# Kernel tuning notes

Hardware: AMD Instinct MI355X
Metric: run time of the kernel (lower is better)

The kernel has to match this reference:

```python
import jax, jax.numpy as jnp
import numpy as np

NUM_BLOCKS = 10  # labels 1..10; label 0 = background
EPS = 1e-6


def setup_inputs() -> dict:
    key = jax.random.key(0)
    k1, k2, k3 = jax.random.split(key, 3)
    shape = (8, 128, 128, 128)
    inp = jax.random.uniform(k1, shape, dtype=jnp.float32)
    tgt = jax.random.uniform(k2, shape, dtype=jnp.float32)
    blk = jax.random.randint(k3, shape, 0, NUM_BLOCKS + 1, dtype=jnp.int32)
    return {"input": inp, "target": tgt, "block": blk}


def _dice_from_sums(intersect, input_area, target_area):
    # intersect/areas: [B, NUM_BLOCKS]; faithful to cal_dice_loss per block.
    denom = input_area + target_area + 2.0 * EPS
    batch_loss = 1.0 - 2.0 * intersect / denom          # [B, NUM_BLOCKS]
    batch_loss = jnp.where(target_area == 0, 0.0, batch_loss)
    valid = jnp.sum(target_area != 0, axis=0).astype(batch_loss.dtype)  # [NUM_BLOCKS]
    return jnp.sum(batch_loss, axis=0) / jnp.maximum(valid, 1.0)        # [NUM_BLOCKS]


def reference(input, target, block):
    B = input.shape[0]
    x = input.reshape(B, -1)
    t = target.reshape(B, -1)
    s = block.reshape(B, -1)

    # One fused pass: per-batch segmented sums over block ids 0..NUM_BLOCKS.
    seg = jax.vmap(lambda v, ids: jax.ops.segment_sum(v, ids, num_segments=NUM_BLOCKS + 1))
    intersect = seg(x * t, s)[:, 1:]   # [B, 10] sum(input*target) within each block
    input_area = seg(x, s)[:, 1:]      # [B, 10]
    target_area = seg(t, s)[:, 1:]     # [B, 10]

    loss_per_block = _dice_from_sums(intersect, input_area, target_area)  # [10]

    # block_tmp.max() != 0  <=>  label b+1 appears anywhere in the tensor
    counts = jnp.sum(s[..., None] == jnp.arange(1, NUM_BLOCKS + 1), axis=(0, 1))
    present = counts > 0                                                   # [10]
    num = jnp.sum(present).astype(loss_per_block.dtype)
    loss = jnp.sum(jnp.where(present, loss_per_block, 0.0)) / num
    return (loss, 0)
```

## Files before the change

### kernel.cpp

```cpp
#include <hip/hip_runtime.h>

#define NB 10
#define BATCH 8
#define EPSF 1e-6f

constexpr int THREADS        = 256;
constexpr int VEC_PER_BATCH  = (128 * 128 * 128) / 4;
constexpr int BLOCKS_PER_BATCH = 64;
constexpr int GRID           = BLOCKS_PER_BATCH * BATCH;
constexpr int WAVE_VEC       = 2048;
constexpr int STAGES         = WAVE_VEC / 64;
constexpr int REC = 32;

__device__ __forceinline__ void dma16(const void* g, void* l) {
    __builtin_amdgcn_global_load_lds(
        (const __attribute__((address_space(1))) void*)g,
        (__attribute__((address_space(3))) void*)l, 16, 0, 0);
}

__global__ __launch_bounds__(THREADS)
void dice_partial(const float* __restrict__ x,
                  const float* __restrict__ t,
                  const int*   __restrict__ s,
                  float* __restrict__ ws)
{
    __shared__ float4 lx[4][4][64];
    __shared__ float4 lt[4][4][64];
    __shared__ int4   lsb[4][4][64];

    const int tid  = threadIdx.x;
    const int wave = tid >> 6, lane = tid & 63;
    const int batch = blockIdx.x >> 6;
    const int sub   = blockIdx.x & 63;
    const long long chunk = (long long)batch * VEC_PER_BATCH
                          + (long long)(sub * 4 + wave) * WAVE_VEC;

    const float4* gx = (const float4*)x + chunk + lane;
    const float4* gt = (const float4*)t + chunk + lane;
    const int4*   gs = (const int4*)s  + chunk + lane;

    float aI[NB], aX[NB], aT[NB];
#pragma unroll
    for (int k = 0; k < NB; ++k) { aI[k] = 0.f; aX[k] = 0.f; aT[k] = 0.f; }
    unsigned bits = 0;

#define DO_ELEM(xe, te, se)                                     \
    do {                                                        \
        const float _x = (xe), _t = (te);                       \
        const int   _s = (se);                                  \
        const float _p = _x * _t;                               \
        bits |= (1u << _s);                                     \
        _Pragma("unroll")                                       \
        for (int k = 0; k < NB; ++k) {                          \
            const float m = (_s == k + 1) ? 1.0f : 0.0f;        \
            aI[k] = fmaf(m, _p, aI[k]);                         \
            aX[k] = fmaf(m, _x, aX[k]);                         \
            aT[k] = fmaf(m, _t, aT[k]);                         \
        }                                                       \
    } while (0)

#pragma unroll
    for (int i = 0; i < 3; ++i) {
        dma16(gx + i * 64, &lx[wave][i][0]);
        dma16(gt + i * 64, &lt[wave][i][0]);
        dma16(gs + i * 64, &lsb[wave][i][0]);
    }
    const float4* px = gx + 3 * 64;
    const float4* pt = gt + 3 * 64;
    const int4*   ps = gs + 3 * 64;

#pragma unroll 1
    for (int i = 0; i < STAGES; ++i) {
        if (i <= STAGES - 3)      asm volatile("s_waitcnt vmcnt(6)" ::: "memory");
        else if (i == STAGES - 2) asm volatile("s_waitcnt vmcnt(3)" ::: "memory");
        else                      asm volatile("s_waitcnt vmcnt(0)" ::: "memory");
        __builtin_amdgcn_sched_barrier(0);

        if (i < STAGES - 3) {
            const int nb = (i + 3) & 3;
            dma16(px, &lx[wave][nb][0]);
            dma16(pt, &lt[wave][nb][0]);
            dma16(ps, &lsb[wave][nb][0]);
            px += 64; pt += 64; ps += 64;
        }

        const int b = i & 3;
        const float4 xv = lx[wave][b][lane];
        const float4 tv = lt[wave][b][lane];
        const int4   sv = lsb[wave][b][lane];
        DO_ELEM(xv.x, tv.x, sv.x);
        DO_ELEM(xv.y, tv.y, sv.y);
        DO_ELEM(xv.z, tv.z, sv.z);
        DO_ELEM(xv.w, tv.w, sv.w);
    }
#undef DO_ELEM

#pragma unroll
    for (int k = 0; k < NB; ++k) {
#pragma unroll
        for (int off = 32; off > 0; off >>= 1) {
            aI[k] += __shfl_xor(aI[k], off);
            aX[k] += __shfl_xor(aX[k], off);
            aT[k] += __shfl_xor(aT[k], off);
        }
    }
#pragma unroll
    for (int off = 32; off > 0; off >>= 1)
        bits |= (unsigned)__shfl_xor((int)bits, off);

    __shared__ float    wsum[4][32];
    __shared__ unsigned wb[4];
    if (lane < NB) {
        wsum[wave][lane]          = aI[lane];
        wsum[wave][NB + lane]     = aX[lane];
        wsum[wave][2 * NB + lane] = aT[lane];
    }
    if (lane == 0) wb[wave] = bits;
    __syncthreads();

    if (tid < 3 * NB) {
        const float v = wsum[0][tid] + wsum[1][tid] + wsum[2][tid] + wsum[3][tid];
        ws[blockIdx.x * REC + tid] = v;
    }
    if (tid == 0)
        ((unsigned*)ws)[blockIdx.x * REC + 30] = wb[0] | wb[1] | wb[2] | wb[3];
}

__global__ void dice_final(const float* __restrict__ ws, float* __restrict__ out)
{
    const int tid = threadIdx.x;
    __shared__ float    sAll[BATCH][3 * NB];
    __shared__ unsigned um[THREADS];

    if (tid < BATCH * 3 * NB) {
        const int batch = tid / (3 * NB);
        const int idx   = tid % (3 * NB);
        float v = 0.0f;
        for (int j = 0; j < BLOCKS_PER_BATCH; ++j)
            v += ws[(batch * BLOCKS_PER_BATCH + j) * REC + idx];
        sAll[batch][idx] = v;
    }

    unsigned m = 0;
#pragma unroll
    for (int j = 0; j < GRID / THREADS; ++j)
        m |= ((const unsigned*)ws)[(tid * (GRID / THREADS) + j) * REC + 30];
    um[tid] = m;
    __syncthreads();
    for (int st = THREADS / 2; st > 0; st >>= 1) {
        if (tid < st) um[tid] |= um[tid + st];
        __syncthreads();
    }
    const unsigned mask = um[0];

    if (tid < 64) {
        float lpb = 0.0f, pres = 0.0f;
        if (tid < NB) {
            float sum_loss = 0.0f, valid = 0.0f;
            for (int b = 0; b < BATCH; ++b) {
                const float I = sAll[b][tid];
                const float X = sAll[b][NB + tid];
                const float T = sAll[b][2 * NB + tid];
                const float denom = X + T + 2.0f * EPSF;
                float bl = 1.0f - 2.0f * I / denom;
                if (T == 0.0f) bl = 0.0f; else valid += 1.0f;
                sum_loss += bl;
            }
            lpb  = sum_loss / fmaxf(valid, 1.0f);
            pres = ((mask >> (tid + 1)) & 1u) ? 1.0f : 0.0f;
        }
        float num = pres;
        float ls  = (pres > 0.0f) ? lpb : 0.0f;
#pragma unroll
        for (int off = 32; off > 0; off >>= 1) {
            num += __shfl_down(num, off);
            ls  += __shfl_down(ls,  off);
        }
        if (tid == 0) {
            out[0] = ls / num;
            out[1] = 0.0f;
        }
    }
}

extern "C" void kernel_launch(void* const* d_in, const int* in_sizes, int n_in,
                              void* d_out, int out_size, void* d_ws, size_t ws_size,
                              hipStream_t stream)
{
    const float* x = (const float*)d_in[0];
    const float* t = (const float*)d_in[1];
    const int*   s = (const int*)d_in[2];
    float* out = (float*)d_out;
    float* ws  = (float*)d_ws;

    dice_partial<<<GRID, THREADS, 0, stream>>>(x, t, s, ws);
    dice_final<<<1, THREADS, 0, stream>>>(ws, out);
}
```

Measured before the change: 45.66 us.

## Deepen LDS DMA ring to six stages and transpose partial-sum workspace layout

```diff
diff --git a/kernel.cpp b/kernel.cpp
--- a/kernel.cpp
+++ b/kernel.cpp
@@ -10,7 +10,8 @@
 constexpr int GRID           = BLOCKS_PER_BATCH * BATCH;
 constexpr int WAVE_VEC       = 2048;
 constexpr int STAGES         = WAVE_VEC / 64;
-constexpr int REC = 32;
+constexpr int RING           = 6;
+
 
 __device__ __forceinline__ void dma16(const void* g, void* l) {
     __builtin_amdgcn_global_load_lds(
@@ -24,9 +25,9 @@
                   const int*   __restrict__ s,
                   float* __restrict__ ws)
 {
-    __shared__ float4 lx[4][4][64];
-    __shared__ float4 lt[4][4][64];
-    __shared__ int4   lsb[4][4][64];
+    __shared__ float4 lx[4][RING][64];
+    __shared__ float4 lt[4][RING][64];
+    __shared__ int4   lsb[4][RING][64];
 
     const int tid  = threadIdx.x;
     const int wave = tid >> 6, lane = tid & 63;
@@ -60,31 +61,33 @@
     } while (0)
 
 #pragma unroll
-    for (int i = 0; i < 3; ++i) {
+    for (int i = 0; i < 5; ++i) {
         dma16(gx + i * 64, &lx[wave][i][0]);
         dma16(gt + i * 64, &lt[wave][i][0]);
         dma16(gs + i * 64, &lsb[wave][i][0]);
     }
-    const float4* px = gx + 3 * 64;
-    const float4* pt = gt + 3 * 64;
-    const int4*   ps = gs + 3 * 64;
+    const float4* px = gx + 5 * 64;
+    const float4* pt = gt + 5 * 64;
+    const int4*   ps = gs + 5 * 64;
 
 #pragma unroll 1
     for (int i = 0; i < STAGES; ++i) {
-        if (i <= STAGES - 3)      asm volatile("s_waitcnt vmcnt(6)" ::: "memory");
-        else if (i == STAGES - 2) asm volatile("s_waitcnt vmcnt(3)" ::: "memory");
-        else                      asm volatile("s_waitcnt vmcnt(0)" ::: "memory");
+        if (i <= STAGES - 5)      asm volatile("s_waitcnt vmcnt(12)" ::: "memory");
+        else if (i == STAGES - 4) asm volatile("s_waitcnt vmcnt(9)"  ::: "memory");
+        else if (i == STAGES - 3) asm volatile("s_waitcnt vmcnt(6)"  ::: "memory");
+        else if (i == STAGES - 2) asm volatile("s_waitcnt vmcnt(3)"  ::: "memory");
+        else                      asm volatile("s_waitcnt vmcnt(0)"  ::: "memory");
         __builtin_amdgcn_sched_barrier(0);
 
-        if (i < STAGES - 3) {
-            const int nb = (i + 3) & 3;
+        if (i < STAGES - 5) {
+            const int nb = (i + 5) % RING;
             dma16(px, &lx[wave][nb][0]);
             dma16(pt, &lt[wave][nb][0]);
             dma16(ps, &lsb[wave][nb][0]);
             px += 64; pt += 64; ps += 64;
         }
 
-        const int b = i & 3;
+        const int b = i % RING;
         const float4 xv = lx[wave][b][lane];
         const float4 tv = lt[wave][b][lane];
         const int4   sv = lsb[wave][b][lane];
@@ -120,32 +123,35 @@
 
     if (tid < 3 * NB) {
         const float v = wsum[0][tid] + wsum[1][tid] + wsum[2][tid] + wsum[3][tid];
-        ws[blockIdx.x * REC + tid] = v;
+        ws[tid * GRID + blockIdx.x] = v;
     }
     if (tid == 0)
-        ((unsigned*)ws)[blockIdx.x * REC + 30] = wb[0] | wb[1] | wb[2] | wb[3];
+        ((unsigned*)ws)[3 * NB * GRID + blockIdx.x] = wb[0] | wb[1] | wb[2] | wb[3];
 }
 
 __global__ void dice_final(const float* __restrict__ ws, float* __restrict__ out)
 {
     const int tid = threadIdx.x;
-    __shared__ float    sAll[BATCH][3 * NB];
+    __shared__ float    sums[BATCH * 3 * NB];
     __shared__ unsigned um[THREADS];
 
-    if (tid < BATCH * 3 * NB) {
-        const int batch = tid / (3 * NB);
-        const int idx   = tid % (3 * NB);
-        float v = 0.0f;
-        for (int j = 0; j < BLOCKS_PER_BATCH; ++j)
-            v += ws[(batch * BLOCKS_PER_BATCH + j) * REC + idx];
-        sAll[batch][idx] = v;
-    }
-
-    unsigned m = 0;
-#pragma unroll
-    for (int j = 0; j < GRID / THREADS; ++j)
-        m |= ((const unsigned*)ws)[(tid * (GRID / THREADS) + j) * REC + 30];
-    um[tid] = m;
+    const int grp = tid >> 4, l16 = tid & 15;
+#pragma unroll
+    for (int j = 0; j < 15; ++j) {
+        const int c = grp + 16 * j;
+        const int batch = c / (3 * NB);
+        const int idx   = c % (3 * NB);
+        const float4 v4 = *(const float4*)&ws[idx * GRID + batch * BLOCKS_PER_BATCH + l16 * 4];
+        float v = v4.x + v4.y + v4.z + v4.w;
+        v += __shfl_xor(v, 8);
+        v += __shfl_xor(v, 4);
+        v += __shfl_xor(v, 2);
+        v += __shfl_xor(v, 1);
+        if (l16 == 0) sums[c] = v;
+    }
+
+    const unsigned* mrow = (const unsigned*)ws + 3 * NB * GRID;
+    um[tid] = mrow[tid] | mrow[tid + 256];
     __syncthreads();
     for (int st = THREADS / 2; st > 0; st >>= 1) {
         if (tid < st) um[tid] |= um[tid + st];
@@ -158,9 +164,9 @@
         if (tid < NB) {
             float sum_loss = 0.0f, valid = 0.0f;
             for (int b = 0; b < BATCH; ++b) {
-                const float I = sAll[b][tid];
-                const float X = sAll[b][NB + tid];
-                const float T = sAll[b][2 * NB + tid];
+                const float I = sums[b * 3 * NB + tid];
+                const float X = sums[b * 3 * NB + NB + tid];
+                const float T = sums[b * 3 * NB + 2 * NB + tid];
                 const float denom = X + T + 2.0f * EPSF;
                 float bl = 1.0f - 2.0f * I / denom;
                 if (T == 0.0f) bl = 0.0f; else valid += 1.0f;
```

New measurement: 51.84 us. 1.14x slower.
